# Optimization experiments

Measured on AMD Instinct MI355X. Metric: run time of the kernel, lower is better.

Reference implementation:

```python
import jax, jax.numpy as jnp
import numpy as np

N, E = 100000, 1600000          # nodes, edges
H, DH = 8, 256                  # heads, dim_hidden
D = DH // H                     # dim per head
NEG_SLOPE = 0.2                 # GAT leaky_relu slope
BETA = 0.5


def setup_inputs() -> dict:
    key = jax.random.key(0)
    ks = jax.random.split(key, 10)
    s = 1.0 / np.sqrt(DH)
    return {
        "x": jax.random.normal(ks[0], (N, DH), jnp.float32),
        "edge_index": jax.random.randint(ks[1], (2, E), 0, N, jnp.int32),
        "edge_attr": jax.random.uniform(ks[2], (E,), jnp.float32),
        # GAT params (no bias, add_self_loops=False)
        "Wg": jax.random.normal(ks[3], (DH, DH), jnp.float32) * s,
        "att_src": jax.random.normal(ks[4], (H, D), jnp.float32) * s,
        "att_dst": jax.random.normal(ks[5], (H, D), jnp.float32) * s,
        # h_lin
        "Wh": jax.random.normal(ks[6], (DH, DH), jnp.float32) * s,
        "bh": jnp.zeros((DH,), jnp.float32),
        # lin
        "Wl": jax.random.normal(ks[7], (DH, DH), jnp.float32) * s,
        "bl": jnp.zeros((DH,), jnp.float32),
        # LayerNorm
        "ln_g": jnp.ones((DH,), jnp.float32),
        "ln_b": jnp.zeros((DH,), jnp.float32),
        # beta gate (beta>=0 -> constant vector)
        "b_param": jnp.full((DH,), BETA, jnp.float32),
    }


def _layer_norm(v, g, b, eps=1e-5):
    mu = jnp.mean(v, axis=-1, keepdims=True)
    var = jnp.var(v, axis=-1, keepdims=True)
    return (v - mu) * jax.lax.rsqrt(var + eps) * g + b


def _weighted_gat(x, edge_index, edge_attr, Wg, att_src, att_dst):
    # GATConv with per-edge weights folded into the softmax numerator.
    xs = (x @ Wg).reshape(N, H, D)                       # [N,H,D]
    a_src = jnp.einsum("nhd,hd->nh", xs, att_src)        # [N,H]
    a_dst = jnp.einsum("nhd,hd->nh", xs, att_dst)
    src, dst = edge_index[0], edge_index[1]
    e = jax.nn.leaky_relu(a_src[src] + a_dst[dst], NEG_SLOPE)   # [E,H]
    m = jax.ops.segment_max(e, dst, num_segments=N)             # [N,H]
    m = jnp.where(jnp.isfinite(m), m, 0.0)                      # isolated nodes
    p = jnp.exp(e - m[dst]) * edge_attr[:, None]                # weighted exp
    denom = jax.ops.segment_sum(p, dst, num_segments=N)         # [N,H]
    alpha = p / (denom[dst] + 1e-16)                            # [E,H]
    msg = alpha[:, :, None] * xs[src]                           # [E,H,D]
    out = jax.ops.segment_sum(msg, dst, num_segments=N)         # [N,H,D]
    return out.reshape(N, DH)


def reference(x, edge_index, edge_attr, Wg, att_src, att_dst, Wh, bh, Wl, bl, ln_g, ln_b, b_param):
    x_in = x
    h = jax.nn.relu(x @ Wh + bh)
    xg = _weighted_gat(x, edge_index, edge_attr, Wg, att_src, att_dst) + (x @ Wl + bl)
    xg = jax.nn.relu(xg)                                  # dropout p=0 (eval)
    beta = b_param[None, :]
    out = (1.0 - beta) * _layer_norm(h * xg, ln_g, ln_b) + beta * xg
    return out + x_in                                     # residual=True
```

## Files before the change

kernel.cpp:

```cpp
#include <hip/hip_runtime.h>

typedef __attribute__((ext_vector_type(4))) float f32x4;
typedef __attribute__((ext_vector_type(8))) __bf16 bf16x8;

__device__ __forceinline__ unsigned short f2bf(float f) {
    return __builtin_bit_cast(unsigned short, (__bf16)f);
}
__device__ __forceinline__ float bf2f(unsigned short u) {
    return __builtin_bit_cast(float, (unsigned)u << 16);
}

__device__ __forceinline__ void gload16(const void* g, void* l) {
    __builtin_amdgcn_global_load_lds(
        (const __attribute__((address_space(1))) void*)g,
        (__attribute__((address_space(3))) void*)l, 16, 0, 0);
}

__global__ __launch_bounds__(256) void k_cvt_x(const float* __restrict__ x,
                                               unsigned short* __restrict__ xb,
                                               long total, long totalPad) {
    long i = ((long)blockIdx.x * 256 + threadIdx.x) * 4;
    if (i >= totalPad) return;
    if (i < total) {
        float4 v = *(const float4*)(x + i);
        ushort4 u;
        u.x = f2bf(v.x); u.y = f2bf(v.y); u.z = f2bf(v.z); u.w = f2bf(v.w);
        *(ushort4*)(xb + i) = u;
    } else {
        ushort4 u = {0, 0, 0, 0};
        *(ushort4*)(xb + i) = u;
    }
}

__global__ __launch_bounds__(256) void k_wt(const float* __restrict__ Wg,
                                            const float* __restrict__ Wh,
                                            const float* __restrict__ Wl,
                                            unsigned short* __restrict__ wt) {
    int t = blockIdx.x * 256 + threadIdx.x;
    int nn = t >> 8, k = t & 255;
    const float* W = (nn < 256) ? Wg : (nn < 512) ? Wh : Wl;
    int c = nn & 255;
    wt[t] = f2bf(W[k * 256 + c]);
}

__global__ __launch_bounds__(256) void k_gemm(
    const unsigned short* __restrict__ A,
    const unsigned short* __restrict__ BT,
    unsigned short* __restrict__ xs, unsigned short* __restrict__ hb,
    unsigned short* __restrict__ xlb,
    const float* __restrict__ bh, const float* __restrict__ bl, int M, int nwg) {
    __shared__ unsigned short Al[128 * 32];
    __shared__ unsigned short Bl[128 * 32];
    const int bid = blockIdx.x;
    const int xcd = bid & 7, idx = bid >> 3;
    const int q = nwg >> 3, r = nwg & 7;
    const int wg = (xcd < r ? xcd * (q + 1) : r * (q + 1) + (xcd - r) * q) + idx;
    const int tm = wg / 6, tn = wg % 6;

    const int tid = threadIdx.x;
    const int lane = tid & 63;
    const int wave = tid >> 6;
    const int wm = (wave >> 1) * 64, wn = (wave & 1) * 64;

    f32x4 acc[4][4] = {};

    const int r0 = tid >> 2;
    const int ce = (tid & 3) * 8;
    const unsigned short* Ag = A + (size_t)tm * 128 * 256 + (size_t)r0 * 256 + ce;
    const unsigned short* Bg = BT + (size_t)tn * 128 * 256 + (size_t)r0 * 256 + ce;

    const int fr = lane & 15;
    const int ko = (lane >> 4) * 8;

    for (int ks = 0; ks < 8; ++ks) {
        const int k0 = ks * 32;
#pragma unroll
        for (int s = 0; s < 2; ++s) {
            gload16(Ag + (size_t)s * 64 * 256 + k0, (char*)Al + s * 4096 + wave * 1024);
            gload16(Bg + (size_t)s * 64 * 256 + k0, (char*)Bl + s * 4096 + wave * 1024);
        }
        __syncthreads();
        bf16x8 af[4], bfr[4];
#pragma unroll
        for (int i = 0; i < 4; ++i) {
            af[i]  = *(const bf16x8*)&Al[(wm + i * 16 + fr) * 32 + ko];
            bfr[i] = *(const bf16x8*)&Bl[(wn + i * 16 + fr) * 32 + ko];
        }
#pragma unroll
        for (int i = 0; i < 4; ++i)
#pragma unroll
            for (int j = 0; j < 4; ++j)
                acc[i][j] = __builtin_amdgcn_mfma_f32_16x16x32_bf16(af[i], bfr[j], acc[i][j], 0, 0, 0);
        __syncthreads();
    }

    const int colbase = tn * 128 + wn;
    const int rbase = tm * 128 + wm + (lane >> 4) * 4;
#pragma unroll
    for (int i = 0; i < 4; ++i) {
#pragma unroll
        for (int j = 0; j < 4; ++j) {
            const int cg = colbase + j * 16 + (lane & 15);
#pragma unroll
            for (int q2 = 0; q2 < 4; ++q2) {
                const int rg = rbase + i * 16 + q2;
                if (rg < M) {
                    float v = acc[i][j][q2];
                    if (cg < 256) {
                        xs[(size_t)rg * 256 + cg] = f2bf(v);
                    } else if (cg < 512) {
                        float t = v + bh[cg - 256];
                        hb[(size_t)rg * 256 + (cg - 256)] = f2bf(t > 0.f ? t : 0.f);
                    } else {
                        xlb[(size_t)rg * 256 + (cg - 512)] = f2bf(v + bl[cg - 512]);
                    }
                }
            }
        }
    }
}

__global__ __launch_bounds__(256) void k_attn(const unsigned short* __restrict__ xs,
                                              const float* __restrict__ att_src,
                                              const float* __restrict__ att_dst,
                                              float* __restrict__ a_src,
                                              float* __restrict__ a_dst, int N) {
    int t = blockIdx.x * 256 + threadIdx.x;
    int n = t >> 3, hh = t & 7;
    if (n >= N) return;
    const ushort4* xp = (const ushort4*)(xs + (size_t)n * 256 + hh * 32);
    const float4* sp = (const float4*)(att_src + hh * 32);
    const float4* dp = (const float4*)(att_dst + hh * 32);
    float sa = 0.f, sd = 0.f;
#pragma unroll
    for (int q = 0; q < 8; ++q) {
        ushort4 u = xp[q];
        float4 s = sp[q], d = dp[q];
        float v0 = bf2f(u.x), v1 = bf2f(u.y), v2 = bf2f(u.z), v3 = bf2f(u.w);
        sa += v0 * s.x + v1 * s.y + v2 * s.z + v3 * s.w;
        sd += v0 * d.x + v1 * d.y + v2 * d.z + v3 * d.w;
    }
    a_src[t] = sa;
    a_dst[t] = sd;
}

__global__ void k_hist(const int* __restrict__ dst, int E, int* __restrict__ deg) {
    for (int e = blockIdx.x * blockDim.x + threadIdx.x; e < E; e += gridDim.x * blockDim.x)
        atomicAdd(&deg[dst[e]], 1);
}

__global__ __launch_bounds__(256) void k_scan1(const int* __restrict__ deg, int* __restrict__ offs,
                                               int* __restrict__ bsum, int Npad) {
    __shared__ int s[256];
    int t = threadIdx.x;
    int i = blockIdx.x * 256 + t;
    int v = (i < Npad) ? deg[i] : 0;
    s[t] = v;
    __syncthreads();
#pragma unroll
    for (int off = 1; off < 256; off <<= 1) {
        int x = (t >= off) ? s[t - off] : 0;
        __syncthreads();
        s[t] += x;
        __syncthreads();
    }
    offs[i] = s[t] - v;
    if (t == 255) bsum[blockIdx.x] = s[255];
}

__global__ __launch_bounds__(512) void k_scan2(int* __restrict__ bsum, int nb) {
    __shared__ int s[512];
    int t = threadIdx.x;
    int v = (t < nb) ? bsum[t] : 0;
    s[t] = v;
    __syncthreads();
#pragma unroll
    for (int off = 1; off < 512; off <<= 1) {
        int x = (t >= off) ? s[t - off] : 0;
        __syncthreads();
        s[t] += x;
        __syncthreads();
    }
    if (t < nb) bsum[t] = s[t] - v;
}

__global__ __launch_bounds__(256) void k_scan3(int* __restrict__ offs, const int* __restrict__ bsum,
                                               int* __restrict__ cursor) {
    int i = blockIdx.x * 256 + threadIdx.x;
    int o = offs[i] + bsum[blockIdx.x];
    offs[i] = o;
    cursor[i] = o;
}

__global__ void k_scatter(const int* __restrict__ ei, const float* __restrict__ ea, int E,
                          int* __restrict__ cursor, int2* __restrict__ csr) {
    for (int e = blockIdx.x * blockDim.x + threadIdx.x; e < E; e += gridDim.x * blockDim.x) {
        int d = ei[(size_t)E + e];
        int pos = atomicAdd(&cursor[d], 1);
        int2 sw;
        sw.x = ei[e];
        sw.y = __builtin_bit_cast(int, ea[e]);
        csr[pos] = sw;
    }
}

__global__ __launch_bounds__(256) void k_agg(
    const int* __restrict__ offs, const int* __restrict__ deg,
    const int2* __restrict__ csr,
    const float* __restrict__ a_src, const float* __restrict__ a_dst,
    const unsigned short* __restrict__ xs, const unsigned short* __restrict__ hb,
    const unsigned short* __restrict__ xlb,
    const float* __restrict__ x, const float* __restrict__ ln_g, const float* __restrict__ ln_b,
    const float* __restrict__ beta, float* __restrict__ out, int N) {
    const int wave = threadIdx.x >> 6, lane = threadIdx.x & 63;
    const int n = blockIdx.x * 4 + wave;
    if (n >= N) return;
    const int start = offs[n];
    const int dcount = deg[n];
    const int head = lane >> 3;
    const int eSub = lane & 7;
    const float adst = a_dst[n * 8 + head];

    f32x4 acc = {0.f, 0.f, 0.f, 0.f};
    float dsum = 0.f;
    const unsigned short* xrow = xs + (size_t)lane * 4;

    for (int g = 0; g < dcount; g += 8) {
        const int eIdx = g + eSub;
        int src = 0;
        float w = 0.f;
        if (eIdx < dcount) {
            int2 sw = csr[start + eIdx];
            src = sw.x;
            w = __builtin_bit_cast(float, sw.y);
        }
        float a = a_src[src * 8 + head] + adst;
        a = (a > 0.f) ? a : 0.2f * a;
        const float pv = __expf(a) * w;
        dsum += pv;

        ushort4 rows[8];
#pragma unroll
        for (int e = 0; e < 8; ++e) {
            const int s = __shfl(src, e);
            rows[e] = *(const ushort4*)(xrow + (size_t)s * 256);
        }
#pragma unroll
        for (int e = 0; e < 8; ++e) {
            const float p = __shfl(pv, (lane & 56) + e);
            acc[0] += p * bf2f(rows[e].x);
            acc[1] += p * bf2f(rows[e].y);
            acc[2] += p * bf2f(rows[e].z);
            acc[3] += p * bf2f(rows[e].w);
        }
    }
    dsum += __shfl_xor(dsum, 1);
    dsum += __shfl_xor(dsum, 2);
    dsum += __shfl_xor(dsum, 4);
    const float inv = 1.f / (dsum + 1e-16f);

    const size_t base = (size_t)n * 256 + lane * 4;
    ushort4 xlu = *(const ushort4*)(xlb + base);
    ushort4 hu = *(const ushort4*)(hb + base);
    f32x4 xg, t4;
    float s1 = 0.f, s2 = 0.f;
    const float xl0[4] = {bf2f(xlu.x), bf2f(xlu.y), bf2f(xlu.z), bf2f(xlu.w)};
    const float hv0[4] = {bf2f(hu.x), bf2f(hu.y), bf2f(hu.z), bf2f(hu.w)};
#pragma unroll
    for (int q = 0; q < 4; ++q) {
        float gg = acc[q] * inv + xl0[q];
        gg = gg > 0.f ? gg : 0.f;
        xg[q] = gg;
        float t = hv0[q] * gg;
        t4[q] = t;
        s1 += t;
        s2 += t * t;
    }
#pragma unroll
    for (int off = 32; off; off >>= 1) {
        s1 += __shfl_xor(s1, off);
        s2 += __shfl_xor(s2, off);
    }
    const float mu = s1 * (1.f / 256.f);
    const float var = s2 * (1.f / 256.f) - mu * mu;
    const float rs = rsqrtf(var + 1e-5f);

    f32x4 g4 = *(const f32x4*)(ln_g + lane * 4);
    f32x4 b4 = *(const f32x4*)(ln_b + lane * 4);
    f32x4 be = *(const f32x4*)(beta + lane * 4);
    f32x4 xin = *(const f32x4*)(x + base);
    f32x4 o;
#pragma unroll
    for (int q = 0; q < 4; ++q) {
        float ln = (t4[q] - mu) * rs * g4[q] + b4[q];
        o[q] = (1.f - be[q]) * ln + be[q] * xg[q] + xin[q];
    }
    *(f32x4*)(out + base) = o;
}

extern "C" void kernel_launch(void* const* d_in, const int* in_sizes, int n_in,
                              void* d_out, int out_size, void* d_ws, size_t ws_size,
                              hipStream_t stream) {
    const float* x = (const float*)d_in[0];
    const int* ei = (const int*)d_in[1];
    const float* ea = (const float*)d_in[2];
    const float* Wg = (const float*)d_in[3];
    const float* att_src = (const float*)d_in[4];
    const float* att_dst = (const float*)d_in[5];
    const float* Wh = (const float*)d_in[6];
    const float* bh = (const float*)d_in[7];
    const float* Wl = (const float*)d_in[8];
    const float* bl = (const float*)d_in[9];
    const float* ln_g = (const float*)d_in[10];
    const float* ln_b = (const float*)d_in[11];
    const float* beta = (const float*)d_in[12];
    float* out = (float*)d_out;

    const int DH = 256;
    const int N = in_sizes[0] / DH;
    const int E = in_sizes[2];
    const int Mpad = ((N + 127) / 128) * 128;
    const int Npad = ((N + 255) / 256) * 256;
    const int nscanb = Npad / 256;
    const int nwg = (Mpad / 128) * 6;

    char* w = (char*)d_ws;
    auto take = [&](size_t bytes) -> char* {
        char* p = w;
        w += (bytes + 255) & ~(size_t)255;
        return p;
    };
    unsigned short* xs = (unsigned short*)take((size_t)N * DH * 2);
    unsigned short* hb = (unsigned short*)take((size_t)N * DH * 2);
    unsigned short* xlb = (unsigned short*)take((size_t)N * DH * 2);
    float* a_src = (float*)take((size_t)N * 8 * 4);
    float* a_dst = (float*)take((size_t)N * 8 * 4);
    unsigned short* xbf = (unsigned short*)take((size_t)Mpad * DH * 2);
    unsigned short* wt = (unsigned short*)take((size_t)768 * 256 * 2);
    int* deg = (int*)take((size_t)Npad * 4);
    int* offs = (int*)take((size_t)Npad * 4);
    int* cursor = (int*)take((size_t)Npad * 4);
    int* bsum = (int*)take(512 * 4);
    int2* csr = (int2*)take((size_t)E * 8);

    hipMemsetAsync(deg, 0, (size_t)Npad * 4, stream);

    k_cvt_x<<<Mpad / 4, 256, 0, stream>>>(x, xbf, (long)N * DH, (long)Mpad * DH);
    k_wt<<<768, 256, 0, stream>>>(Wg, Wh, Wl, wt);

    k_hist<<<2048, 256, 0, stream>>>(ei + E, E, deg);
    k_scan1<<<nscanb, 256, 0, stream>>>(deg, offs, bsum, Npad);
    k_scan2<<<1, 512, 0, stream>>>(bsum, nscanb);
    k_scan3<<<nscanb, 256, 0, stream>>>(offs, bsum, cursor);
    k_scatter<<<2048, 256, 0, stream>>>(ei, ea, E, cursor, csr);

    k_gemm<<<nwg, 256, 0, stream>>>(xbf, wt, xs, hb, xlb, bh, bl, N, nwg);

    k_attn<<<(N * 8 + 255) / 256, 256, 0, stream>>>(xs, att_src, att_dst, a_src, a_dst, N);

    k_agg<<<(N + 3) / 4, 256, 0, stream>>>(offs, deg, csr, a_src, a_dst,
                                           xs, hb, xlb, x, ln_g, ln_b, beta, out, N);
}
```

Measured before the change: 585.2 us.

## Fuse prep kernels and precompute per-edge attention weights during CSR scatter

Merges x conversion, weight transpose and degree histogram into one launch. Moves the scatter after the attention-score kernel so it computes the leaky-relu, exp and edge-weight product for all 8 heads per edge, storing them as bf16 next to the source index in CSR order. The aggregation kernel then reads precomputed weights instead of gathering a_src per edge and recomputing exp. This adds a 16-byte-per-edge write and read, and rounds the softmax numerators to bf16.

```diff
diff --git a/kernel.cpp b/kernel.cpp
--- a/kernel.cpp
+++ b/kernel.cpp
@@ -16,31 +16,36 @@
         (__attribute__((address_space(3))) void*)l, 16, 0, 0);
 }
 
-__global__ __launch_bounds__(256) void k_cvt_x(const float* __restrict__ x,
-                                               unsigned short* __restrict__ xb,
-                                               long total, long totalPad) {
-    long i = ((long)blockIdx.x * 256 + threadIdx.x) * 4;
-    if (i >= totalPad) return;
-    if (i < total) {
-        float4 v = *(const float4*)(x + i);
-        ushort4 u;
-        u.x = f2bf(v.x); u.y = f2bf(v.y); u.z = f2bf(v.z); u.w = f2bf(v.w);
-        *(ushort4*)(xb + i) = u;
+__global__ __launch_bounds__(256) void k_prep(
+    const float* __restrict__ x, unsigned short* __restrict__ xb, long total, long totalPad,
+    const float* __restrict__ Wg, const float* __restrict__ Wh, const float* __restrict__ Wl,
+    unsigned short* __restrict__ wt,
+    const int* __restrict__ dst, int E, int* __restrict__ deg,
+    int nCvt, int nHist) {
+    const int b = blockIdx.x;
+    const int tid = threadIdx.x;
+    if (b < nCvt) {
+        long i = ((long)b * 256 + tid) * 4;
+        if (i >= totalPad) return;
+        if (i < total) {
+            float4 v = *(const float4*)(x + i);
+            ushort4 u;
+            u.x = f2bf(v.x); u.y = f2bf(v.y); u.z = f2bf(v.z); u.w = f2bf(v.w);
+            *(ushort4*)(xb + i) = u;
+        } else {
+            ushort4 u = {0, 0, 0, 0};
+            *(ushort4*)(xb + i) = u;
+        }
+    } else if (b < nCvt + 768) {
+        int t = (b - nCvt) * 256 + tid;
+        int nn = t >> 8, k = t & 255;
+        const float* W = (nn < 256) ? Wg : (nn < 512) ? Wh : Wl;
+        wt[t] = f2bf(W[k * 256 + (nn & 255)]);
     } else {
-        ushort4 u = {0, 0, 0, 0};
-        *(ushort4*)(xb + i) = u;
-    }
-}
-
-__global__ __launch_bounds__(256) void k_wt(const float* __restrict__ Wg,
-                                            const float* __restrict__ Wh,
-                                            const float* __restrict__ Wl,
-                                            unsigned short* __restrict__ wt) {
-    int t = blockIdx.x * 256 + threadIdx.x;
-    int nn = t >> 8, k = t & 255;
-    const float* W = (nn < 256) ? Wg : (nn < 512) ? Wh : Wl;
-    int c = nn & 255;
-    wt[t] = f2bf(W[k * 256 + c]);
+        int bb = b - nCvt - 768;
+        for (int e = bb * 256 + tid; e < E; e += nHist * 256)
+            atomicAdd(&deg[dst[e]], 1);
+    }
 }
 
 __global__ __launch_bounds__(256) void k_gemm(
@@ -144,11 +149,6 @@
     a_dst[t] = sd;
 }
 
-__global__ void k_hist(const int* __restrict__ dst, int E, int* __restrict__ deg) {
-    for (int e = blockIdx.x * blockDim.x + threadIdx.x; e < E; e += gridDim.x * blockDim.x)
-        atomicAdd(&deg[dst[e]], 1);
-}
-
 __global__ __launch_bounds__(256) void k_scan1(const int* __restrict__ deg, int* __restrict__ offs,
                                                int* __restrict__ bsum, int Npad) {
     __shared__ int s[256];
@@ -192,22 +192,39 @@
     cursor[i] = o;
 }
 
-__global__ void k_scatter(const int* __restrict__ ei, const float* __restrict__ ea, int E,
-                          int* __restrict__ cursor, int2* __restrict__ csr) {
+__global__ void k_edge(const int* __restrict__ ei, const float* __restrict__ ea, int E,
+                       const float* __restrict__ a_src, const float* __restrict__ a_dst,
+                       int* __restrict__ cursor, int* __restrict__ srcArr,
+                       unsigned short* __restrict__ pvArr) {
     for (int e = blockIdx.x * blockDim.x + threadIdx.x; e < E; e += gridDim.x * blockDim.x) {
-        int d = ei[(size_t)E + e];
-        int pos = atomicAdd(&cursor[d], 1);
-        int2 sw;
-        sw.x = ei[e];
-        sw.y = __builtin_bit_cast(int, ea[e]);
-        csr[pos] = sw;
+        const int s = ei[e];
+        const int d = ei[(size_t)E + e];
+        const float w = ea[e];
+        const int pos = atomicAdd(&cursor[d], 1);
+        const float4* As = (const float4*)(a_src + (size_t)s * 8);
+        const float4* Ad = (const float4*)(a_dst + (size_t)d * 8);
+        float4 s0 = As[0], s1 = As[1], d0 = Ad[0], d1 = Ad[1];
+        float a[8] = {s0.x + d0.x, s0.y + d0.y, s0.z + d0.z, s0.w + d0.w,
+                      s1.x + d1.x, s1.y + d1.y, s1.z + d1.z, s1.w + d1.w};
+        unsigned pk[4];
+#pragma unroll
+        for (int h = 0; h < 4; ++h) {
+            float lo = a[2 * h], hi = a[2 * h + 1];
+            lo = (lo > 0.f) ? lo : 0.2f * lo;
+            hi = (hi > 0.f) ? hi : 0.2f * hi;
+            unsigned short plo = f2bf(__expf(lo) * w);
+            unsigned short phi = f2bf(__expf(hi) * w);
+            pk[h] = (unsigned)plo | ((unsigned)phi << 16);
+        }
+        srcArr[pos] = s;
+        uint4 v = {pk[0], pk[1], pk[2], pk[3]};
+        *(uint4*)(pvArr + (size_t)pos * 8) = v;
     }
 }
 
 __global__ __launch_bounds__(256) void k_agg(
     const int* __restrict__ offs, const int* __restrict__ deg,
-    const int2* __restrict__ csr,
-    const float* __restrict__ a_src, const float* __restrict__ a_dst,
+    const int* __restrict__ srcArr, const unsigned short* __restrict__ pvArr,
     const unsigned short* __restrict__ xs, const unsigned short* __restrict__ hb,
     const unsigned short* __restrict__ xlb,
     const float* __restrict__ x, const float* __restrict__ ln_g, const float* __restrict__ ln_b,
@@ -219,7 +236,6 @@
     const int dcount = deg[n];
     const int head = lane >> 3;
     const int eSub = lane & 7;
-    const float adst = a_dst[n * 8 + head];
 
     f32x4 acc = {0.f, 0.f, 0.f, 0.f};
     float dsum = 0.f;
@@ -227,16 +243,13 @@
 
     for (int g = 0; g < dcount; g += 8) {
         const int eIdx = g + eSub;
+        const bool act = eIdx < dcount;
         int src = 0;
-        float w = 0.f;
-        if (eIdx < dcount) {
-            int2 sw = csr[start + eIdx];
-            src = sw.x;
-            w = __builtin_bit_cast(float, sw.y);
-        }
-        float a = a_src[src * 8 + head] + adst;
-        a = (a > 0.f) ? a : 0.2f * a;
-        const float pv = __expf(a) * w;
+        float pv = 0.f;
+        if (act) {
+            src = srcArr[start + eIdx];
+            pv = bf2f(pvArr[(size_t)(start + eIdx) * 8 + head]);
+        }
         dsum += pv;
 
         ushort4 rows[8];
@@ -323,6 +336,8 @@
     const int Npad = ((N + 255) / 256) * 256;
     const int nscanb = Npad / 256;
     const int nwg = (Mpad / 128) * 6;
+    const int nCvt = Mpad / 4;
+    const int nHist = 2048;
 
     char* w = (char*)d_ws;
     auto take = [&](size_t bytes) -> char* {
@@ -341,23 +356,24 @@
     int* offs = (int*)take((size_t)Npad * 4);
     int* cursor = (int*)take((size_t)Npad * 4);
     int* bsum = (int*)take(512 * 4);
-    int2* csr = (int2*)take((size_t)E * 8);
+    int* srcArr = (int*)take((size_t)E * 4);
+    unsigned short* pvArr = (unsigned short*)take((size_t)E * 8 * 2);
 
     hipMemsetAsync(deg, 0, (size_t)Npad * 4, stream);
 
-    k_cvt_x<<<Mpad / 4, 256, 0, stream>>>(x, xbf, (long)N * DH, (long)Mpad * DH);
-    k_wt<<<768, 256, 0, stream>>>(Wg, Wh, Wl, wt);
-
-    k_hist<<<2048, 256, 0, stream>>>(ei + E, E, deg);
+    k_prep<<<nCvt + 768 + nHist, 256, 0, stream>>>(x, xbf, (long)N * DH, (long)Mpad * DH,
+                                                   Wg, Wh, Wl, wt, ei + E, E, deg, nCvt, nHist);
+
     k_scan1<<<nscanb, 256, 0, stream>>>(deg, offs, bsum, Npad);
     k_scan2<<<1, 512, 0, stream>>>(bsum, nscanb);
     k_scan3<<<nscanb, 256, 0, stream>>>(offs, bsum, cursor);
-    k_scatter<<<2048, 256, 0, stream>>>(ei, ea, E, cursor, csr);
 
     k_gemm<<<nwg, 256, 0, stream>>>(xbf, wt, xs, hb, xlb, bh, bl, N, nwg);
 
     k_attn<<<(N * 8 + 255) / 256, 256, 0, stream>>>(xs, att_src, att_dst, a_src, a_dst, N);
 
-    k_agg<<<(N + 3) / 4, 256, 0, stream>>>(offs, deg, csr, a_src, a_dst,
+    k_edge<<<2048, 256, 0, stream>>>(ei, ea, E, a_src, a_dst, cursor, srcArr, pvArr);
+
+    k_agg<<<(N + 3) / 4, 256, 0, stream>>>(offs, deg, srcArr, pvArr,
                                            xs, hb, xlb, x, ln_g, ln_b, beta, out, N);
 }
```

After: 561.9 us. -4.0%, faster.
